# Optimization experiments

Measured on AMD Instinct MI355X. Metric: run time of the kernel, lower is better.

## Reference

```python
import jax, jax.numpy as jnp
import numpy as np

N_NODES = 50000
N_EDGES = 800000
INDIM = 128
HIDIM = 128
OUTDIM = 128


def setup_inputs() -> dict:
    key = jax.random.key(0)
    ks = jax.random.split(key, 12)
    x = jax.random.normal(ks[0], (N_NODES, INDIM), dtype=jnp.float32)
    edge_index = jax.random.randint(ks[1], (2, N_EDGES), 0, N_NODES, dtype=jnp.int64)
    edge_weights = jax.random.normal(ks[2], (N_EDGES, 1), dtype=jnp.float32)
    # GINEConv internal edge projection Linear(1 -> feat_dim) per layer
    We1 = jax.random.normal(ks[3], (1, INDIM), dtype=jnp.float32)
    be1 = jnp.zeros((INDIM,), dtype=jnp.float32)
    # layer MLPs (nn.Linear)
    W1 = jax.random.normal(ks[4], (INDIM, HIDIM), dtype=jnp.float32) / np.sqrt(INDIM)
    b1 = jnp.zeros((HIDIM,), dtype=jnp.float32)
    We2 = jax.random.normal(ks[5], (1, HIDIM), dtype=jnp.float32)
    be2 = jnp.zeros((HIDIM,), dtype=jnp.float32)
    W2 = jax.random.normal(ks[6], (HIDIM, OUTDIM), dtype=jnp.float32) / np.sqrt(HIDIM)
    b2 = jnp.zeros((OUTDIM,), dtype=jnp.float32)
    return {"x": x, "edge_index": edge_index, "edge_weights": edge_weights,
            "We1": We1, "be1": be1, "W1": W1, "b1": b1,
            "We2": We2, "be2": be2, "W2": W2, "b2": b2}


def _gine_conv(h, src, dst, edge_attr, We, be, W, b):
    # edge embedding: Linear(1 -> d)
    e = edge_attr @ We + be                     # [E, d]
    # message: relu(x_j + e_ij), gather from source nodes
    msg = jax.nn.relu(h[src] + e)               # [E, d]
    # scatter-sum aggregate at destination nodes
    agg = jax.ops.segment_sum(msg, dst, num_segments=N_NODES)  # [N, d]
    # (1 + eps) * x + aggr, eps = 0 (PyG default), then nn (Linear)
    return (h + agg) @ W + b


def reference(x, edge_index, edge_weights, We1, be1, W1, b1, We2, be2, W2, b2):
    src = edge_index[0]
    dst = edge_index[1]
    h = jax.nn.relu(_gine_conv(x, src, dst, edge_weights, We1, be1, W1, b1))
    out = _gine_conv(h, src, dst, edge_weights, We2, be2, W2, b2)
    return out
```

## Files before the change

kernel.cpp:

```cpp
#include <hip/hip_runtime.h>


typedef unsigned long long u64;
typedef unsigned int u32;
typedef unsigned short ushort;
typedef __attribute__((ext_vector_type(8))) short short8;
typedef __attribute__((ext_vector_type(4))) float f32x4;
typedef __attribute__((ext_vector_type(2))) float f32x2;
typedef __attribute__((ext_vector_type(4))) u32 u32x4;

constexpr int NN = 50000;
constexpr int NE = 800000;
constexpr int D  = 128;
constexpr int BSH = 6;
constexpr int NB  = (NN + 63) >> BSH;
constexpr int NC  = 128;
constexpr int CHUNK = NE / NC;
constexpr int BCAP = 4096;
constexpr int GR = 32;
constexpr int GG = (NN + GR - 1) / GR;
constexpr int CBLK = NN * D / 8 / 256;

__device__ __forceinline__ ushort f2bf(float f) {
    u32 u = __float_as_uint(f);
    return (ushort)((u + 0x7FFFu + ((u >> 16) & 1u)) >> 16);
}
__device__ __forceinline__ float bfl(u32 u) {
    return __uint_as_float(u << 16);
}
__device__ __forceinline__ float bfh(u32 u) {
    return __uint_as_float(u & 0xFFFF0000u);
}
__device__ __forceinline__ f32x2 unpk(u32 u) {
    f32x2 r; r.x = bfl(u); r.y = bfh(u); return r;
}
__device__ __forceinline__ u64 pack_edge(int src, int d6, float w) {
    return ((u64)__float_as_uint(w) << 32) | (u32)(src | (d6 << 17));
}


__global__ __launch_bounds__(256) void prep_hist(
    const float* __restrict__ x,  ushort* __restrict__ xb,
    const float* __restrict__ W1, const float* __restrict__ W2,
    ushort* __restrict__ Wt1, ushort* __restrict__ Wt2,
    const int* __restrict__ dst, int* __restrict__ G)
{
    int blk = blockIdx.x;
    if (blk < CBLK) {
        int base = (blk * 256 + threadIdx.x) * 8;
        float4 a = *(const float4*)(x + base);
        float4 b = *(const float4*)(x + base + 4);
        uint4 o;
        o.x = (u32)f2bf(a.x) | ((u32)f2bf(a.y) << 16);
        o.y = (u32)f2bf(a.z) | ((u32)f2bf(a.w) << 16);
        o.z = (u32)f2bf(b.x) | ((u32)f2bf(b.y) << 16);
        o.w = (u32)f2bf(b.z) | ((u32)f2bf(b.w) << 16);
        *(uint4*)(xb + base) = o;
    } else if (blk < CBLK + 8) {
        int b = blk - CBLK;
        const float* W  = (b >= 4) ? W2 : W1;
        ushort*      Wt = (b >= 4) ? Wt2 : Wt1;
        int k0 = (b & 3) * 32;
        for (int i = threadIdx.x; i < 32 * D; i += 256) {
            int n = i >> 5, r = i & 31;
            Wt[n * D + k0 + r] = f2bf(W[(k0 + r) * D + n]);
        }
    } else {
        __shared__ int hh[NB];
        int t = threadIdx.x, c = blk - CBLK - 8;
        for (int i = t; i < NB; i += 256) hh[i] = 0;
        __syncthreads();
        int e0 = c * CHUNK;
        for (int i = t; i < CHUNK; i += 256)
            atomicAdd(&hh[dst[e0 + i] >> BSH], 1);
        __syncthreads();
        for (int i = t; i < NB; i += 256) G[c * NB + i] = hh[i];
    }
}


__global__ __launch_bounds__(1024) void scan_bases(
    const int* __restrict__ G, int* __restrict__ P, int* __restrict__ B)
{
    __shared__ int tsum[1024];
    int t = threadIdx.x;
    int S = 0;
    if (t < NB) {
        #pragma unroll 4
        for (int cc = 0; cc < NC; ++cc) S += G[cc * NB + t];
    }
    tsum[t] = S;
    __syncthreads();
    for (int d = 1; d < 1024; d <<= 1) {
        int v = (t >= d) ? tsum[t - d] : 0;
        __syncthreads();
        tsum[t] += v;
        __syncthreads();
    }
    if (t < NB) {
        int run = tsum[t] - S;
        B[t] = run;
        #pragma unroll 4
        for (int cc = 0; cc < NC; ++cc) {
            P[cc * NB + t] = run;
            run += G[cc * NB + t];
        }
    }
    if (t == 0) B[NB] = NE;
}


__global__ __launch_bounds__(1024) void bucket_scatter(
    const int*   __restrict__ src,
    const int*   __restrict__ dst,
    const float* __restrict__ ew,
    const int*   __restrict__ P,
    u64*         __restrict__ stage)
{
    __shared__ int base_s[NB];
    __shared__ int cnt_s[NB];
    const int t = threadIdx.x, c = blockIdx.x;
    for (int i = t; i < NB; i += 1024) {
        base_s[i] = P[c * NB + i];
        cnt_s[i] = 0;
    }
    __syncthreads();
    int e0 = c * CHUNK;
    for (int i = t; i < CHUNK; i += 1024) {
        int e  = e0 + i;
        int d  = dst[e];
        int bk = d >> BSH;
        int r  = atomicAdd(&cnt_s[bk], 1);
        stage[base_s[bk] + r] = pack_edge(src[e], d & 63, ew[e]);
    }
}

__global__ __launch_bounds__(256) void bucket_csr(
    const int* __restrict__ B, u64* __restrict__ stage, int* __restrict__ off)
{
    __shared__ u64 buf[BCAP];
    __shared__ int cnt[64];
    __shared__ int cur[64];
    __shared__ int noff[64];
    int t = threadIdx.x, b = blockIdx.x;
    int e0 = B[b], e1 = B[b + 1];
    int n = e1 - e0;
    if (n > BCAP) n = BCAP;
    if (t < 64) { cnt[t] = 0; cur[t] = 0; }
    __syncthreads();
    for (int i = t; i < n; i += 256)
        atomicAdd(&cnt[(int)((stage[e0 + i] >> 17) & 63)], 1);
    __syncthreads();
    if (t == 0) {
        int run = 0;
        for (int j = 0; j < 64; ++j) { noff[j] = run; run += cnt[j]; }
    }
    __syncthreads();
    int n0 = b << BSH;
    if (t < 64 && (n0 + t) < NN) off[n0 + t] = e0 + noff[t];
    if (b == NB - 1 && t == 0) off[NN] = NE;
    for (int i = t; i < n; i += 256) {
        u64 p = stage[e0 + i];
        int d6 = (int)((p >> 17) & 63);
        int r = atomicAdd(&cur[d6], 1);
        buf[noff[d6] + r] = p;
    }
    __syncthreads();
    for (int i = t; i < n; i += 256) stage[e0 + i] = buf[i];
}


__global__ __launch_bounds__(256, 4) void gine_layer(
    const ushort* __restrict__ hb,
    const int*    __restrict__ off,
    const u64*    __restrict__ epk,
    const float*  __restrict__ We,
    const float*  __restrict__ be,
    const ushort* __restrict__ Wtb,
    const float*  __restrict__ bias,
    float*        __restrict__ outf,
    ushort*       __restrict__ outb,
    int relu)
{
    __shared__ ushort As[GR * 140];

    const int t    = threadIdx.x;
    const int row0 = blockIdx.x * GR;

    const int g  = t >> 4;
    const int d8 = (t & 15) << 3;

    f32x2 wv[4], bv[4];
    #pragma unroll
    for (int j = 0; j < 4; ++j) {
        wv[j] = *(const f32x2*)(We + d8 + 2 * j);
        bv[j] = *(const f32x2*)(be + d8 + 2 * j);
    }
    const f32x2 zero2 = {0.f, 0.f};

    for (int nrep = 0; nrep < GR / 16; ++nrep) {
        int ln = nrep * 16 + g;
        int n  = row0 + ln;
        f32x2 a[4] = {zero2, zero2, zero2, zero2};
        if (n < NN) {
            u32x4 sv = *(const u32x4*)(hb + (size_t)n * D + d8);
            int e0 = off[n], e1 = off[n + 1];
            u64 p[8];
            int m0 = e1 - e0; if (m0 > 8) m0 = 8;
            #pragma unroll
            for (int k = 0; k < 8; ++k) p[k] = (k < m0) ? epk[e0 + k] : 0;
            for (int e = e0; e < e1; e += 8) {
                int m = e1 - e; if (m > 8) m = 8;
                u32x4 hv[8];
                #pragma unroll
                for (int k = 0; k < 8; ++k)
                    hv[k] = *(const u32x4*)(hb + (size_t)(p[k] & 0x1FFFF) * D + d8);
                u64 pn[8];
                int mn = e1 - (e + 8); if (mn > 8) mn = 8;
                #pragma unroll
                for (int k = 0; k < 8; ++k)
                    pn[k] = (k < mn) ? epk[e + 8 + k] : 0;
                #pragma unroll
                for (int k = 0; k < 8; ++k) {
                    if (k < m) {
                        float w = __uint_as_float((u32)(p[k] >> 32));
                        f32x2 w2 = {w, w};
                        a[0] += __builtin_elementwise_max(zero2,
                                  unpk(hv[k].x) + __builtin_elementwise_fma(w2, wv[0], bv[0]));
                        a[1] += __builtin_elementwise_max(zero2,
                                  unpk(hv[k].y) + __builtin_elementwise_fma(w2, wv[1], bv[1]));
                        a[2] += __builtin_elementwise_max(zero2,
                                  unpk(hv[k].z) + __builtin_elementwise_fma(w2, wv[2], bv[2]));
                        a[3] += __builtin_elementwise_max(zero2,
                                  unpk(hv[k].w) + __builtin_elementwise_fma(w2, wv[3], bv[3]));
                    }
                }
                #pragma unroll
                for (int k = 0; k < 8; ++k) p[k] = pn[k];
            }
            a[0] += unpk(sv.x);
            a[1] += unpk(sv.y);
            a[2] += unpk(sv.z);
            a[3] += unpk(sv.w);
        }
        uint2 lo, hi;
        lo.x = (u32)f2bf(a[0].x) | ((u32)f2bf(a[0].y) << 16);
        lo.y = (u32)f2bf(a[1].x) | ((u32)f2bf(a[1].y) << 16);
        hi.x = (u32)f2bf(a[2].x) | ((u32)f2bf(a[2].y) << 16);
        hi.y = (u32)f2bf(a[3].x) | ((u32)f2bf(a[3].y) << 16);
        *(uint2*)&As[ln * 140 + d8]     = lo;
        *(uint2*)&As[ln * 140 + d8 + 4] = hi;
    }
    __syncthreads();

    const int wave = t >> 6;
    const int lane = t & 63;
    const int q    = lane >> 4;
    const int m    = lane & 15;
    const int wc   = wave * 32;

    f32x4 acc[2][2] = {};
    #pragma unroll
    for (int kb = 0; kb < 4; ++kb) {
        int ak = kb * 32 + q * 8;
        short8 af[2];
        #pragma unroll
        for (int rg = 0; rg < 2; ++rg)
            af[rg] = *(const short8*)&As[(rg * 16 + m) * 140 + ak];
        #pragma unroll
        for (int ct = 0; ct < 2; ++ct) {
            short8 bf = *(const short8*)(Wtb + (wc + ct * 16 + m) * D + ak);
            #pragma unroll
            for (int rg = 0; rg < 2; ++rg)
                acc[rg][ct] = __builtin_amdgcn_mfma_f32_16x16x32_bf16(
                    af[rg], bf, acc[rg][ct], 0, 0, 0);
        }
    }

    #pragma unroll
    for (int ct = 0; ct < 2; ++ct) {
        int col = wc + ct * 16 + m;
        float bc = bias[col];
        #pragma unroll
        for (int rg = 0; rg < 2; ++rg) {
            #pragma unroll
            for (int r = 0; r < 4; ++r) {
                int grow = row0 + rg * 16 + q * 4 + r;
                if (grow < NN) {
                    float v = acc[rg][ct][r] + bc;
                    if (relu) v = fmaxf(0.f, v);
                    if (outb) outb[(size_t)grow * D + col] = f2bf(v);
                    else __builtin_nontemporal_store(v, outf + (size_t)grow * D + col);
                }
            }
        }
    }
}

extern "C" void kernel_launch(void* const* d_in, const int* in_sizes, int n_in,
                              void* d_out, int out_size, void* d_ws, size_t ws_size,
                              hipStream_t stream)
{
    const float* x   = (const float*)d_in[0];
    const int*   ei  = (const int*)  d_in[1];
    const float* ew  = (const float*)d_in[2];
    const float* We1 = (const float*)d_in[3];
    const float* be1 = (const float*)d_in[4];
    const float* W1  = (const float*)d_in[5];
    const float* b1  = (const float*)d_in[6];
    const float* We2 = (const float*)d_in[7];
    const float* be2 = (const float*)d_in[8];
    const float* W2  = (const float*)d_in[9];
    const float* b2  = (const float*)d_in[10];

    float* out = (float*)d_out;

    ushort* xb   = (ushort*)d_ws;
    ushort* hb   = xb + (size_t)NN * D;
    ushort* aggb = hb + (size_t)NN * D;
    ushort* Wt1  = aggb + (size_t)NN * D;
    ushort* Wt2  = Wt1 + D * D;
    u64*   stage = (u64*)(Wt2 + D * D);
    int*   G     = (int*)(stage + NE);
    int*   P     = G + NC * NB;
    int*   B     = P + NC * NB;
    int*   off   = B + NB + 2;

    const int* src = ei;
    const int* dst = ei + NE;

    prep_hist<<<CBLK + 8 + NC, 256, 0, stream>>>(x, xb, W1, W2, Wt1, Wt2,
                                                 dst, G);

    scan_bases<<<1, 1024, 0, stream>>>(G, P, B);
    bucket_scatter<<<NC, 1024, 0, stream>>>(src, dst, ew, P, stage);
    bucket_csr<<<NB, 256, 0, stream>>>(B, stage, off);

    gine_layer<<<GG, 256, 0, stream>>>(xb, off, stage, We1, be1, Wt1, b1,
                                       nullptr, hb, 1);

    gine_layer<<<GG, 256, 0, stream>>>(hb, off, stage, We2, be2, Wt2, b2,
                                       out, nullptr, 0);
}
```

Baseline: 228.7 us.

## Replace two-level bucket sort CSR build with global atomic counting sort

```diff
diff --git a/kernel.cpp b/kernel.cpp
--- a/kernel.cpp
+++ b/kernel.cpp
@@ -12,14 +12,12 @@
 constexpr int NN = 50000;
 constexpr int NE = 800000;
 constexpr int D  = 128;
-constexpr int BSH = 6;
-constexpr int NB  = (NN + 63) >> BSH;
 constexpr int NC  = 128;
 constexpr int CHUNK = NE / NC;
-constexpr int BCAP = 4096;
 constexpr int GR = 32;
 constexpr int GG = (NN + GR - 1) / GR;
 constexpr int CBLK = NN * D / 8 / 256;
+constexpr int SCB = (NN + 1023) / 1024;
 
 __device__ __forceinline__ ushort f2bf(float f) {
     u32 u = __float_as_uint(f);
@@ -33,9 +31,6 @@
 }
 __device__ __forceinline__ f32x2 unpk(u32 u) {
     f32x2 r; r.x = bfl(u); r.y = bfh(u); return r;
-}
-__device__ __forceinline__ u64 pack_edge(int src, int d6, float w) {
-    return ((u64)__float_as_uint(w) << 32) | (u32)(src | (d6 << 17));
 }
 
 
@@ -43,7 +38,7 @@
     const float* __restrict__ x,  ushort* __restrict__ xb,
     const float* __restrict__ W1, const float* __restrict__ W2,
     ushort* __restrict__ Wt1, ushort* __restrict__ Wt2,
-    const int* __restrict__ dst, int* __restrict__ G)
+    const int* __restrict__ dst, int* __restrict__ cnt)
 {
     int blk = blockIdx.x;
     if (blk < CBLK) {
@@ -66,107 +61,67 @@
             Wt[n * D + k0 + r] = f2bf(W[(k0 + r) * D + n]);
         }
     } else {
-        __shared__ int hh[NB];
         int t = threadIdx.x, c = blk - CBLK - 8;
-        for (int i = t; i < NB; i += 256) hh[i] = 0;
-        __syncthreads();
         int e0 = c * CHUNK;
         for (int i = t; i < CHUNK; i += 256)
-            atomicAdd(&hh[dst[e0 + i] >> BSH], 1);
-        __syncthreads();
-        for (int i = t; i < NB; i += 256) G[c * NB + i] = hh[i];
-    }
-}
-
-
-__global__ __launch_bounds__(1024) void scan_bases(
-    const int* __restrict__ G, int* __restrict__ P, int* __restrict__ B)
-{
-    __shared__ int tsum[1024];
-    int t = threadIdx.x;
-    int S = 0;
-    if (t < NB) {
-        #pragma unroll 4
-        for (int cc = 0; cc < NC; ++cc) S += G[cc * NB + t];
-    }
-    tsum[t] = S;
+            atomicAdd(&cnt[dst[e0 + i]], 1);
+    }
+}
+
+
+__global__ __launch_bounds__(1024) void scan1(
+    const int* __restrict__ cnt, int* __restrict__ off, int* __restrict__ S)
+{
+    __shared__ int ts[1024];
+    int b = blockIdx.x, t = threadIdx.x, i = b * 1024 + t;
+    int v = (i < NN) ? cnt[i] : 0;
+    ts[t] = v;
     __syncthreads();
     for (int d = 1; d < 1024; d <<= 1) {
-        int v = (t >= d) ? tsum[t - d] : 0;
+        int u = (t >= d) ? ts[t - d] : 0;
         __syncthreads();
-        tsum[t] += v;
+        ts[t] += u;
         __syncthreads();
     }
-    if (t < NB) {
-        int run = tsum[t] - S;
-        B[t] = run;
-        #pragma unroll 4
-        for (int cc = 0; cc < NC; ++cc) {
-            P[cc * NB + t] = run;
-            run += G[cc * NB + t];
-        }
-    }
-    if (t == 0) B[NB] = NE;
-}
-
-
-__global__ __launch_bounds__(1024) void bucket_scatter(
+    if (i < NN) off[i] = ts[t] - v;
+    if (t == 1023) S[b] = ts[1023];
+}
+
+
+__global__ __launch_bounds__(1024) void scan2(
+    const int* __restrict__ S, int* __restrict__ off, int* __restrict__ cur)
+{
+    __shared__ int base_s;
+    int b = blockIdx.x, t = threadIdx.x, i = b * 1024 + t;
+    if (t < 64) {
+        int v = (t < b) ? S[t] : 0;
+        #pragma unroll
+        for (int o = 32; o; o >>= 1) v += __shfl_down(v, o, 64);
+        if (t == 0) base_s = v;
+    }
+    __syncthreads();
+    int base = base_s;
+    if (i < NN) {
+        int o = off[i] + base;
+        off[i] = o;
+        cur[i] = o;
+    }
+    if (b == 0 && t == 0) off[NN] = NE;
+}
+
+
+__global__ __launch_bounds__(256) void ticket_scatter(
     const int*   __restrict__ src,
     const int*   __restrict__ dst,
     const float* __restrict__ ew,
-    const int*   __restrict__ P,
+    int*         __restrict__ cur,
     u64*         __restrict__ stage)
 {
-    __shared__ int base_s[NB];
-    __shared__ int cnt_s[NB];
-    const int t = threadIdx.x, c = blockIdx.x;
-    for (int i = t; i < NB; i += 1024) {
-        base_s[i] = P[c * NB + i];
-        cnt_s[i] = 0;
-    }
-    __syncthreads();
-    int e0 = c * CHUNK;
-    for (int i = t; i < CHUNK; i += 1024) {
-        int e  = e0 + i;
-        int d  = dst[e];
-        int bk = d >> BSH;
-        int r  = atomicAdd(&cnt_s[bk], 1);
-        stage[base_s[bk] + r] = pack_edge(src[e], d & 63, ew[e]);
-    }
-}
-
-__global__ __launch_bounds__(256) void bucket_csr(
-    const int* __restrict__ B, u64* __restrict__ stage, int* __restrict__ off)
-{
-    __shared__ u64 buf[BCAP];
-    __shared__ int cnt[64];
-    __shared__ int cur[64];
-    __shared__ int noff[64];
-    int t = threadIdx.x, b = blockIdx.x;
-    int e0 = B[b], e1 = B[b + 1];
-    int n = e1 - e0;
-    if (n > BCAP) n = BCAP;
-    if (t < 64) { cnt[t] = 0; cur[t] = 0; }
-    __syncthreads();
-    for (int i = t; i < n; i += 256)
-        atomicAdd(&cnt[(int)((stage[e0 + i] >> 17) & 63)], 1);
-    __syncthreads();
-    if (t == 0) {
-        int run = 0;
-        for (int j = 0; j < 64; ++j) { noff[j] = run; run += cnt[j]; }
-    }
-    __syncthreads();
-    int n0 = b << BSH;
-    if (t < 64 && (n0 + t) < NN) off[n0 + t] = e0 + noff[t];
-    if (b == NB - 1 && t == 0) off[NN] = NE;
-    for (int i = t; i < n; i += 256) {
-        u64 p = stage[e0 + i];
-        int d6 = (int)((p >> 17) & 63);
-        int r = atomicAdd(&cur[d6], 1);
-        buf[noff[d6] + r] = p;
-    }
-    __syncthreads();
-    for (int i = t; i < n; i += 256) stage[e0 + i] = buf[i];
+    int e = blockIdx.x * 256 + threadIdx.x;
+    if (e >= NE) return;
+    int d = dst[e];
+    int slot = atomicAdd(&cur[d], 1);
+    stage[slot] = ((u64)__float_as_uint(ew[e]) << 32) | (u32)src[e];
 }
 
 
@@ -317,24 +272,27 @@
 
     ushort* xb   = (ushort*)d_ws;
     ushort* hb   = xb + (size_t)NN * D;
-    ushort* aggb = hb + (size_t)NN * D;
-    ushort* Wt1  = aggb + (size_t)NN * D;
+    ushort* Wt1  = hb + (size_t)NN * D;
     ushort* Wt2  = Wt1 + D * D;
     u64*   stage = (u64*)(Wt2 + D * D);
-    int*   G     = (int*)(stage + NE);
-    int*   P     = G + NC * NB;
-    int*   B     = P + NC * NB;
-    int*   off   = B + NB + 2;
+    int*   cnt   = (int*)(stage + NE);
+    int*   off   = cnt + NN;
+    int*   cur   = off + NN + 1;
+    int*   S     = cur + NN;
 
     const int* src = ei;
     const int* dst = ei + NE;
 
+    hipMemsetAsync(cnt, 0, NN * sizeof(int), stream);
+
     prep_hist<<<CBLK + 8 + NC, 256, 0, stream>>>(x, xb, W1, W2, Wt1, Wt2,
-                                                 dst, G);
-
-    scan_bases<<<1, 1024, 0, stream>>>(G, P, B);
-    bucket_scatter<<<NC, 1024, 0, stream>>>(src, dst, ew, P, stage);
-    bucket_csr<<<NB, 256, 0, stream>>>(B, stage, off);
+                                                 dst, cnt);
+
+    scan1<<<SCB, 1024, 0, stream>>>(cnt, off, S);
+    scan2<<<SCB, 1024, 0, stream>>>(S, off, cur);
+
+    ticket_scatter<<<(NE + 255) / 256, 256, 0, stream>>>(src, dst, ew, cur,
+                                                         stage);
 
     gine_layer<<<GG, 256, 0, stream>>>(xb, off, stage, We1, be1, Wt1, b1,
                                        nullptr, hb, 1);
```

New measurement: 275.0 us. 1.2x slower.

## Fuse scan into bucket scatter and move x cast into CSR kernel

Applied to the files above, without the earlier changes.

```diff
diff --git a/kernel.cpp b/kernel.cpp
--- a/kernel.cpp
+++ b/kernel.cpp
@@ -19,7 +19,8 @@
 constexpr int BCAP = 4096;
 constexpr int GR = 32;
 constexpr int GG = (NN + GR - 1) / GR;
-constexpr int CBLK = NN * D / 8 / 256;
+constexpr int NU4 = NN * D / 8;
+constexpr int CPB = 1024;
 
 __device__ __forceinline__ ushort f2bf(float f) {
     u32 u = __float_as_uint(f);
@@ -39,35 +40,15 @@
 }
 
 
-__global__ __launch_bounds__(256) void prep_hist(
-    const float* __restrict__ x,  ushort* __restrict__ xb,
+__global__ __launch_bounds__(256) void hist_w(
     const float* __restrict__ W1, const float* __restrict__ W2,
     ushort* __restrict__ Wt1, ushort* __restrict__ Wt2,
     const int* __restrict__ dst, int* __restrict__ G)
 {
     int blk = blockIdx.x;
-    if (blk < CBLK) {
-        int base = (blk * 256 + threadIdx.x) * 8;
-        float4 a = *(const float4*)(x + base);
-        float4 b = *(const float4*)(x + base + 4);
-        uint4 o;
-        o.x = (u32)f2bf(a.x) | ((u32)f2bf(a.y) << 16);
-        o.y = (u32)f2bf(a.z) | ((u32)f2bf(a.w) << 16);
-        o.z = (u32)f2bf(b.x) | ((u32)f2bf(b.y) << 16);
-        o.w = (u32)f2bf(b.z) | ((u32)f2bf(b.w) << 16);
-        *(uint4*)(xb + base) = o;
-    } else if (blk < CBLK + 8) {
-        int b = blk - CBLK;
-        const float* W  = (b >= 4) ? W2 : W1;
-        ushort*      Wt = (b >= 4) ? Wt2 : Wt1;
-        int k0 = (b & 3) * 32;
-        for (int i = threadIdx.x; i < 32 * D; i += 256) {
-            int n = i >> 5, r = i & 31;
-            Wt[n * D + k0 + r] = f2bf(W[(k0 + r) * D + n]);
-        }
-    } else {
+    if (blk < NC) {
         __shared__ int hh[NB];
-        int t = threadIdx.x, c = blk - CBLK - 8;
+        int t = threadIdx.x, c = blk;
         for (int i = t; i < NB; i += 256) hh[i] = 0;
         __syncthreads();
         int e0 = c * CHUNK;
@@ -75,56 +56,65 @@
             atomicAdd(&hh[dst[e0 + i] >> BSH], 1);
         __syncthreads();
         for (int i = t; i < NB; i += 256) G[c * NB + i] = hh[i];
-    }
-}
-
-
-__global__ __launch_bounds__(1024) void scan_bases(
-    const int* __restrict__ G, int* __restrict__ P, int* __restrict__ B)
-{
+    } else {
+        int b = blk - NC;
+        const float* W  = (b >= 4) ? W2 : W1;
+        ushort*      Wt = (b >= 4) ? Wt2 : Wt1;
+        int k0 = (b & 3) * 32;
+        for (int i = threadIdx.x; i < 32 * D; i += 256) {
+            int n = i >> 5, r = i & 31;
+            Wt[n * D + k0 + r] = f2bf(W[(k0 + r) * D + n]);
+        }
+    }
+}
+
+
+__global__ __launch_bounds__(1024) void bucket_scatter(
+    const int*   __restrict__ src,
+    const int*   __restrict__ dst,
+    const float* __restrict__ ew,
+    const int*   __restrict__ G,
+    int*         __restrict__ B,
+    u64*         __restrict__ stage)
+{
+    __shared__ int base_s[NB];
+    __shared__ int cnt_s[NB];
+    __shared__ int pre_s[NB];
     __shared__ int tsum[1024];
-    int t = threadIdx.x;
-    int S = 0;
+    const int t = threadIdx.x, c = blockIdx.x;
+
+    int S = 0, P = 0;
     if (t < NB) {
-        #pragma unroll 4
-        for (int cc = 0; cc < NC; ++cc) S += G[cc * NB + t];
+        #pragma unroll 8
+        for (int cc = 0; cc < NC; ++cc) {
+            int g = G[cc * NB + t];
+            S += g;
+            if (cc < c) P += g;
+        }
+        pre_s[t] = P;
     }
     tsum[t] = S;
     __syncthreads();
+
     for (int d = 1; d < 1024; d <<= 1) {
         int v = (t >= d) ? tsum[t - d] : 0;
         __syncthreads();
         tsum[t] += v;
         __syncthreads();
     }
+    if (t < NB) base_s[t] = tsum[t] - S;
+    __syncthreads();
+
+    if (c == 0) {
+        if (t < NB) B[t] = base_s[t];
+        if (t == 0) B[NB] = NE;
+    }
     if (t < NB) {
-        int run = tsum[t] - S;
-        B[t] = run;
-        #pragma unroll 4
-        for (int cc = 0; cc < NC; ++cc) {
-            P[cc * NB + t] = run;
-            run += G[cc * NB + t];
-        }
-    }
-    if (t == 0) B[NB] = NE;
-}
-
-
-__global__ __launch_bounds__(1024) void bucket_scatter(
-    const int*   __restrict__ src,
-    const int*   __restrict__ dst,
-    const float* __restrict__ ew,
-    const int*   __restrict__ P,
-    u64*         __restrict__ stage)
-{
-    __shared__ int base_s[NB];
-    __shared__ int cnt_s[NB];
-    const int t = threadIdx.x, c = blockIdx.x;
-    for (int i = t; i < NB; i += 1024) {
-        base_s[i] = P[c * NB + i];
-        cnt_s[i] = 0;
-    }
-    __syncthreads();
+        base_s[t] += pre_s[t];
+        cnt_s[t] = 0;
+    }
+    __syncthreads();
+
     int e0 = c * CHUNK;
     for (int i = t; i < CHUNK; i += 1024) {
         int e  = e0 + i;
@@ -135,14 +125,32 @@
     }
 }
 
-__global__ __launch_bounds__(256) void bucket_csr(
-    const int* __restrict__ B, u64* __restrict__ stage, int* __restrict__ off)
+__global__ __launch_bounds__(256) void bucket_csr_cast(
+    const int* __restrict__ B, u64* __restrict__ stage, int* __restrict__ off,
+    const float* __restrict__ x, ushort* __restrict__ xb)
 {
     __shared__ u64 buf[BCAP];
     __shared__ int cnt[64];
     __shared__ int cur[64];
     __shared__ int noff[64];
     int t = threadIdx.x, b = blockIdx.x;
+
+    #pragma unroll
+    for (int j = 0; j < CPB / 256; ++j) {
+        int i = b * CPB + j * 256 + t;
+        if (i < NU4) {
+            int base = i * 8;
+            float4 a = *(const float4*)(x + base);
+            float4 c = *(const float4*)(x + base + 4);
+            uint4 o;
+            o.x = (u32)f2bf(a.x) | ((u32)f2bf(a.y) << 16);
+            o.y = (u32)f2bf(a.z) | ((u32)f2bf(a.w) << 16);
+            o.z = (u32)f2bf(c.x) | ((u32)f2bf(c.y) << 16);
+            o.w = (u32)f2bf(c.z) | ((u32)f2bf(c.w) << 16);
+            *(uint4*)(xb + base) = o;
+        }
+    }
+
     int e0 = B[b], e1 = B[b + 1];
     int n = e1 - e0;
     if (n > BCAP) n = BCAP;
@@ -317,24 +325,20 @@
 
     ushort* xb   = (ushort*)d_ws;
     ushort* hb   = xb + (size_t)NN * D;
-    ushort* aggb = hb + (size_t)NN * D;
-    ushort* Wt1  = aggb + (size_t)NN * D;
+    ushort* Wt1  = hb + (size_t)NN * D;
     ushort* Wt2  = Wt1 + D * D;
     u64*   stage = (u64*)(Wt2 + D * D);
     int*   G     = (int*)(stage + NE);
-    int*   P     = G + NC * NB;
-    int*   B     = P + NC * NB;
+    int*   B     = G + NC * NB;
     int*   off   = B + NB + 2;
 
     const int* src = ei;
     const int* dst = ei + NE;
 
-    prep_hist<<<CBLK + 8 + NC, 256, 0, stream>>>(x, xb, W1, W2, Wt1, Wt2,
-                                                 dst, G);
-
-    scan_bases<<<1, 1024, 0, stream>>>(G, P, B);
-    bucket_scatter<<<NC, 1024, 0, stream>>>(src, dst, ew, P, stage);
-    bucket_csr<<<NB, 256, 0, stream>>>(B, stage, off);
+    hist_w<<<NC + 8, 256, 0, stream>>>(W1, W2, Wt1, Wt2, dst, G);
+
+    bucket_scatter<<<NC, 1024, 0, stream>>>(src, dst, ew, G, B, stage);
+    bucket_csr_cast<<<NB, 256, 0, stream>>>(B, stage, off, x, xb);
 
     gine_layer<<<GG, 256, 0, stream>>>(xb, off, stage, We1, be1, Wt1, b1,
                                        nullptr, hb, 1);
```

Result: faster. 209.4 us (-8.5%).
